# Kernel tuning notes

Measured on AMD Instinct MI355X. Metric: run time of the kernel, lower is better.

The kernel has to match this reference:

```python
import jax, jax.numpy as jnp
import numpy as np

N, E = 100000, 1600000
NF, HC, NC = 32, 64, 64


def setup_inputs() -> dict:
    key = jax.random.key(0)
    ks = jax.random.split(key, 12)
    s = 0.05
    return {
        "x": jax.random.normal(ks[0], (N, NF), dtype=jnp.float32),
        "edge_index": jax.random.randint(ks[1], (2, E), 0, N, dtype=jnp.int64),
        "eps1": jnp.float32(0.0),
        "eps2": jnp.float32(0.0),
        "W1a": jax.random.normal(ks[2], (NF, HC), dtype=jnp.float32) * s,
        "b1a": jnp.zeros((HC,), dtype=jnp.float32),
        "W1b": jax.random.normal(ks[3], (HC, HC), dtype=jnp.float32) * s,
        "b1b": jnp.zeros((HC,), dtype=jnp.float32),
        "W2a": jax.random.normal(ks[4], (HC, HC), dtype=jnp.float32) * s,
        "b2a": jnp.zeros((HC,), dtype=jnp.float32),
        "W2b": jax.random.normal(ks[5], (HC, NC), dtype=jnp.float32) * s,
        "b2b": jnp.zeros((NC,), dtype=jnp.float32),
    }


def _gin_conv(h, src, dst, eps, Wa, ba, Wb, bb, num_nodes):
    # sum-aggregate neighbor features: out[dst] += h[src]
    agg = jax.ops.segment_sum(h[src], dst, num_segments=num_nodes)
    z = (1.0 + eps) * h + agg
    # 2-layer MLP: Linear -> ReLU -> Linear
    z = jax.nn.relu(z @ Wa + ba)
    return z @ Wb + bb


def reference(x, edge_index, eps1, eps2, W1a, b1a, W1b, b1b, W2a, b2a, W2b, b2b):
    src, dst = edge_index[0], edge_index[1]
    n = x.shape[0]
    emb = _gin_conv(x, src, dst, eps1, W1a, b1a, W1b, b1b, n)  # [N, HC]
    h = jax.nn.relu(emb)  # dropout is identity in eval mode
    logits = _gin_conv(h, src, dst, eps2, W2a, b2a, W2b, b2b, n)  # [N, NC]
    return (logits, emb)
```

## Files before the change

### kernel.cpp

```cpp
#include <hip/hip_runtime.h>


#define NFEAT 32
#define HID   64
#define NCLS  64

#define BSH    6
#define BNODES 64
#define BCAP   2048
#define NBKT_LDS 2048

typedef unsigned int uint;
typedef unsigned short ushortT;
typedef __attribute__((ext_vector_type(8))) short bf16x8;
typedef __attribute__((ext_vector_type(4))) float f32x4;

__device__ __forceinline__ int clampi(int v, int hi){ v = v < 0 ? 0 : v; return v > hi ? hi : v; }

__device__ __forceinline__ ushortT f2b(float f){
  uint u = __float_as_uint(f);
  u = (u + 0x7FFFu + ((u >> 16) & 1u)) >> 16;
  return (ushortT)u;
}
__device__ __forceinline__ float b2f_lo(uint u){ return __uint_as_float(u << 16); }
__device__ __forceinline__ float b2f_hi(uint u){ return __uint_as_float(u & 0xFFFF0000u); }
__device__ __forceinline__ uint pack2(float lo, float hi){
  return (uint)f2b(lo) | ((uint)f2b(hi) << 16);
}


__global__ void k_prep(const float* __restrict__ x, ushortT* __restrict__ xb, int n4,
                       const float* __restrict__ W1a, const float* __restrict__ W1b,
                       const float* __restrict__ W2a, const float* __restrict__ W2b,
                       ushortT* __restrict__ T1a, ushortT* __restrict__ T1b,
                       ushortT* __restrict__ T2a, ushortT* __restrict__ T2b,
                       int* __restrict__ bktCnt, int nbkt){
  int t = blockIdx.x*256 + threadIdx.x;
  if (t < n4){
    float4 v = reinterpret_cast<const float4*>(x)[t];
    ushort4 o = { f2b(v.x), f2b(v.y), f2b(v.z), f2b(v.w) };
    reinterpret_cast<ushort4*>(xb)[t] = o;
  }
  if (t < nbkt) bktCnt[t] = 0;
  if (t < 14336){
    const float* W; ushortT* T; int K; int base;
    if      (t <  2048){ W=W1a; T=T1a; K=32; base=0;     }
    else if (t <  6144){ W=W1b; T=T1b; K=64; base=2048;  }
    else if (t < 10240){ W=W2a; T=T2a; K=64; base=6144;  }
    else               { W=W2b; T=T2b; K=64; base=10240; }
    int o = t - base;
    int k = o >> 6, c = o & 63;
    T[c*K + k] = f2b(W[o]);
  }
}


__global__ void k_bucket(const int* __restrict__ src, const int* __restrict__ dst,
                         int E, int N, int nbkt,
                         int* __restrict__ bktCnt, int* __restrict__ bktData){
  __shared__ int s_cnt[NBKT_LDS];
  __shared__ int s_base[NBKT_LDS];
  const int t = threadIdx.x;
  for (int j = t; j < nbkt; j += 256) s_cnt[j] = 0;
  __syncthreads();

  const int e0 = blockIdx.x * 4096;
  const int e1 = min(e0 + 4096, E);
  for (int e = e0 + t; e < e1; e += 256){
    int d = clampi(dst[e], N-1);
    atomicAdd(&s_cnt[d >> BSH], 1);
  }
  __syncthreads();
  for (int j = t; j < nbkt; j += 256){
    int c = s_cnt[j];
    s_base[j] = (c > 0) ? atomicAdd(&bktCnt[j], c) : 0;
    s_cnt[j] = 0;
  }
  __syncthreads();
  for (int e = e0 + t; e < e1; e += 256){
    int d = clampi(dst[e], N-1);
    int s = clampi(src[e], N-1);
    int b = d >> BSH;
    int p = s_base[b] + atomicAdd(&s_cnt[b], 1);
    if (p < BCAP)
      bktData[(size_t)b * BCAP + p] = ((d & (BNODES-1)) << 17) | s;
  }
}


template<int K, bool WRITE_HB>
__global__ __launch_bounds__(512)
void k_fused(const uint4* __restrict__ f4,
             const int* __restrict__ bktCnt, const int* __restrict__ bktData,
             const float* __restrict__ epsP,
             const ushortT* __restrict__ WaT,
             const float* __restrict__ ba,
             const ushortT* __restrict__ WbT,
             const float* __restrict__ bb,
             float* __restrict__ out,
             ushortT* __restrict__ hb, int N){
  constexpr int RS = K/8;
  constexpr int CH = RS/4;
  constexpr int U  = (CH == 1) ? 4 : 2;
  __shared__ int s_data[BCAP];
  __shared__ int s_eidx[BCAP];
  __shared__ int s_h[BNODES], s_cur[BNODES], s_row[BNODES+1];
  __shared__ __align__(16) ushortT zt[64*K];
  __shared__ __align__(16) ushortT ht[64*64];
  const int t = threadIdx.x;
  const int blk = blockIdx.x;
  const int row0 = blk * 64;

  const int cnt = min(bktCnt[blk], BCAP);
  const int* __restrict__ data = bktData + (size_t)blk * BCAP;
  if (t < BNODES) s_h[t] = 0;
  __syncthreads();
  for (int j = t; j < cnt; j += 512){
    int v = data[j];
    s_data[j] = v;
    atomicAdd(&s_h[v >> 17], 1);
  }
  __syncthreads();
  if (t < BNODES){
    int deg = s_h[t];
    int v = deg;
    #pragma unroll
    for (int off = 1; off < 64; off <<= 1){
      int u = __shfl_up(v, off);
      if (t >= off) v += u;
    }
    s_row[t+1] = v;
    if (t == 0) s_row[0] = 0;
    s_cur[t] = v - deg;
  }
  __syncthreads();
  for (int j = t; j < cnt; j += 512){
    int v = s_data[j];
    int p = atomicAdd(&s_cur[v >> 17], 1);
    s_eidx[p] = v & 0x1FFFF;
  }
  __syncthreads();

  {
    const int n = t >> 3;
    const int L = t & 7;
    const int q = L & 3;
    const int s = L >> 2;
    const int node = row0 + n;
    float acc[CH*8];
    #pragma unroll
    for (int j = 0; j < CH*8; ++j) acc[j] = 0.f;

    const int b = s_row[n];
    const int e = s_row[n+1];
    int i = b + s;
    for (; i + 2*(U-1) < e; i += 2*U){
      int src[U];
      #pragma unroll
      for (int u = 0; u < U; ++u) src[u] = s_eidx[i + 2*u];
      uint4 v[U][CH];
      #pragma unroll
      for (int u = 0; u < U; ++u)
        #pragma unroll
        for (int c = 0; c < CH; ++c)
          v[u][c] = f4[(size_t)src[u]*RS + q*CH + c];
      #pragma unroll
      for (int u = 0; u < U; ++u)
        #pragma unroll
        for (int c = 0; c < CH; ++c){
          acc[c*8+0] += b2f_lo(v[u][c].x); acc[c*8+1] += b2f_hi(v[u][c].x);
          acc[c*8+2] += b2f_lo(v[u][c].y); acc[c*8+3] += b2f_hi(v[u][c].y);
          acc[c*8+4] += b2f_lo(v[u][c].z); acc[c*8+5] += b2f_hi(v[u][c].z);
          acc[c*8+6] += b2f_lo(v[u][c].w); acc[c*8+7] += b2f_hi(v[u][c].w);
        }
    }
    for (; i < e; i += 2){
      int src0 = s_eidx[i];
      #pragma unroll
      for (int c = 0; c < CH; ++c){
        uint4 v = f4[(size_t)src0*RS + q*CH + c];
        acc[c*8+0] += b2f_lo(v.x); acc[c*8+1] += b2f_hi(v.x);
        acc[c*8+2] += b2f_lo(v.y); acc[c*8+3] += b2f_hi(v.y);
        acc[c*8+4] += b2f_lo(v.z); acc[c*8+5] += b2f_hi(v.z);
        acc[c*8+6] += b2f_lo(v.w); acc[c*8+7] += b2f_hi(v.w);
      }
    }
    if (s == 1 && node < N){
      const float se = 1.0f + epsP[0];
      #pragma unroll
      for (int c = 0; c < CH; ++c){
        uint4 v = f4[(size_t)node*RS + q*CH + c];
        acc[c*8+0] = fmaf(se, b2f_lo(v.x), acc[c*8+0]);
        acc[c*8+1] = fmaf(se, b2f_hi(v.x), acc[c*8+1]);
        acc[c*8+2] = fmaf(se, b2f_lo(v.y), acc[c*8+2]);
        acc[c*8+3] = fmaf(se, b2f_hi(v.y), acc[c*8+3]);
        acc[c*8+4] = fmaf(se, b2f_lo(v.z), acc[c*8+4]);
        acc[c*8+5] = fmaf(se, b2f_hi(v.z), acc[c*8+5]);
        acc[c*8+6] = fmaf(se, b2f_lo(v.w), acc[c*8+6]);
        acc[c*8+7] = fmaf(se, b2f_hi(v.w), acc[c*8+7]);
      }
    }
    #pragma unroll
    for (int j = 0; j < CH*8; ++j) acc[j] += __shfl_xor(acc[j], 4);
    if (s == 0){
      #pragma unroll
      for (int c = 0; c < CH; ++c){
        uint4 z;
        z.x = pack2(acc[c*8+0], acc[c*8+1]);
        z.y = pack2(acc[c*8+2], acc[c*8+3]);
        z.z = pack2(acc[c*8+4], acc[c*8+5]);
        z.w = pack2(acc[c*8+6], acc[c*8+7]);
        reinterpret_cast<uint4*>(zt)[n*RS + q*CH + c] = z;
      }
    }
  }
  __syncthreads();

  const int w  = t >> 6;
  const int l  = t & 63;
  const int lr = l & 15;
  const int lg = l >> 4;
  const int rf = w & 3;
  const int c0 = (w >> 2) * 2;
  f32x4 c1[2];
  #pragma unroll
  for (int cl = 0; cl < 2; ++cl){ float bv = ba[(c0+cl)*16 + lr]; c1[cl] = (f32x4){bv,bv,bv,bv}; }
  #pragma unroll
  for (int kf = 0; kf < K/32; ++kf){
    bf16x8 a = *reinterpret_cast<const bf16x8*>(&zt[(rf*16 + lr)*K + kf*32 + lg*8]);
    #pragma unroll
    for (int cl = 0; cl < 2; ++cl){
      bf16x8 bfr = *reinterpret_cast<const bf16x8*>(&WaT[((c0+cl)*16 + lr)*K + kf*32 + lg*8]);
      c1[cl] = __builtin_amdgcn_mfma_f32_16x16x32_bf16(a, bfr, c1[cl], 0, 0, 0);
    }
  }
  #pragma unroll
  for (int cl = 0; cl < 2; ++cl)
    #pragma unroll
    for (int r = 0; r < 4; ++r)
      ht[(rf*16 + lg*4 + r)*64 + (c0+cl)*16 + lr] = f2b(fmaxf(c1[cl][r], 0.f));
  __syncthreads();

  f32x4 c2[2];
  #pragma unroll
  for (int cl = 0; cl < 2; ++cl){ float bv = bb[(c0+cl)*16 + lr]; c2[cl] = (f32x4){bv,bv,bv,bv}; }
  #pragma unroll
  for (int kf = 0; kf < 2; ++kf){
    bf16x8 a = *reinterpret_cast<const bf16x8*>(&ht[(rf*16 + lr)*64 + kf*32 + lg*8]);
    #pragma unroll
    for (int cl = 0; cl < 2; ++cl){
      bf16x8 bfr = *reinterpret_cast<const bf16x8*>(&WbT[((c0+cl)*16 + lr)*64 + kf*32 + lg*8]);
      c2[cl] = __builtin_amdgcn_mfma_f32_16x16x32_bf16(a, bfr, c2[cl], 0, 0, 0);
    }
  }
  #pragma unroll
  for (int cl = 0; cl < 2; ++cl)
    #pragma unroll
    for (int r = 0; r < 4; ++r){
      int row = row0 + rf*16 + lg*4 + r;
      if (row < N){
        float v = c2[cl][r];
        out[(size_t)row*64 + (c0+cl)*16 + lr] = v;
        if (WRITE_HB) hb[(size_t)row*64 + (c0+cl)*16 + lr] = f2b(fmaxf(v, 0.f));
      }
    }
}


extern "C" void kernel_launch(void* const* d_in, const int* in_sizes, int n_in,
                              void* d_out, int out_size, void* d_ws, size_t ws_size,
                              hipStream_t stream) {
  const int N = in_sizes[0] / NFEAT;
  const int E = in_sizes[1] / 2;
  const int nbkt = (N + BNODES - 1) / BNODES;

  const float* x    = (const float*)d_in[0];
  const int*   ei   = (const int*)d_in[1];
  const int*   srcI = ei;
  const int*   dstI = ei + E;
  const float* eps1 = (const float*)d_in[2];
  const float* eps2 = (const float*)d_in[3];
  const float* W1a  = (const float*)d_in[4];
  const float* b1a  = (const float*)d_in[5];
  const float* W1b  = (const float*)d_in[6];
  const float* b1b  = (const float*)d_in[7];
  const float* W2a  = (const float*)d_in[8];
  const float* b2a  = (const float*)d_in[9];
  const float* W2b  = (const float*)d_in[10];
  const float* b2b  = (const float*)d_in[11];

  float* outLogits = (float*)d_out;
  float* outEmb    = outLogits + (size_t)N * HID;

  char* w = (char*)d_ws;
  size_t off = 0;
  auto alloc = [&](size_t bytes) -> void* {
    void* p = w + off;
    off = (off + bytes + 255) & ~(size_t)255;
    return p;
  };
  int*     bktCnt  = (int*)alloc((size_t)nbkt * sizeof(int));
  ushortT* T1a     = (ushortT*)alloc(64*32*sizeof(ushortT));
  ushortT* T1b     = (ushortT*)alloc(64*64*sizeof(ushortT));
  ushortT* T2a     = (ushortT*)alloc(64*64*sizeof(ushortT));
  ushortT* T2b     = (ushortT*)alloc(64*64*sizeof(ushortT));
  int*     bktData = (int*)alloc((size_t)nbkt * BCAP * sizeof(int));
  ushortT* xb      = (ushortT*)alloc((size_t)N * NFEAT * sizeof(ushortT));
  ushortT* hb      = (ushortT*)alloc((size_t)N * HID * sizeof(ushortT));

  const int n4 = N * NFEAT / 4;
  k_prep<<<(n4+255)/256, 256, 0, stream>>>(x, xb, n4, W1a, W1b, W2a, W2b,
                                           T1a, T1b, T2a, T2b, bktCnt, nbkt);

  k_bucket<<<(E+4095)/4096, 256, 0, stream>>>(srcI, dstI, E, N, nbkt, bktCnt, bktData);

  k_fused<NFEAT, true><<<nbkt, 512, 0, stream>>>((const uint4*)xb, bktCnt, bktData,
      eps1, T1a, b1a, T1b, b1b, outEmb, hb, N);

  k_fused<HID, false><<<nbkt, 512, 0, stream>>>((const uint4*)hb, bktCnt, bktData,
      eps2, T2a, b2a, T2b, b2b, outLogits, (ushortT*)nullptr, N);
}
```

Measured before the change: 119.5 us.

## Use coarse 512-node buckets with per-block octant filtering and padded LDS tiles

Buckets in k_bucket now cover 512 destination nodes, so there are far fewer of them (at most 256). Each fused block scans its whole bucket and keeps only the edges whose destination falls in its 64-node octant, using a wave ballot and a shared atomic to compact them. The aim is to cut global atomic contention and scattered writes during bucketing. The cost is that eight blocks each reread the same bucket window. LDS tiles for z and h also get padded row strides to reduce bank conflicts.

```diff
diff --git a/kernel.cpp b/kernel.cpp
--- a/kernel.cpp
+++ b/kernel.cpp
@@ -5,12 +5,14 @@
 #define HID   64
 #define NCLS  64
 
-#define BSH    6
-#define BNODES 64
-#define BCAP   2048
-#define NBKT_LDS 2048
+#define BSH   9
+#define BNODES 512
+#define NBKT_MAX 256
+#define BCAP  16384
+#define ECAP  2048
 
 typedef unsigned int uint;
+typedef unsigned long long ull;
 typedef unsigned short ushortT;
 typedef __attribute__((ext_vector_type(8))) short bf16x8;
 typedef __attribute__((ext_vector_type(4))) float f32x4;
@@ -58,8 +60,8 @@
 __global__ void k_bucket(const int* __restrict__ src, const int* __restrict__ dst,
                          int E, int N, int nbkt,
                          int* __restrict__ bktCnt, int* __restrict__ bktData){
-  __shared__ int s_cnt[NBKT_LDS];
-  __shared__ int s_base[NBKT_LDS];
+  __shared__ int s_cnt[NBKT_MAX];
+  __shared__ int s_base[NBKT_MAX];
   const int t = threadIdx.x;
   for (int j = t; j < nbkt; j += 256) s_cnt[j] = 0;
   __syncthreads();
@@ -102,26 +104,50 @@
   constexpr int RS = K/8;
   constexpr int CH = RS/4;
   constexpr int U  = (CH == 1) ? 4 : 2;
-  __shared__ int s_data[BCAP];
-  __shared__ int s_eidx[BCAP];
-  __shared__ int s_h[BNODES], s_cur[BNODES], s_row[BNODES+1];
-  __shared__ __align__(16) ushortT zt[64*K];
-  __shared__ __align__(16) ushortT ht[64*64];
+  constexpr int ZS = K + 8;
+  constexpr int HS = 72;
+  __shared__ int s_data[ECAP];
+  __shared__ int s_eidx[ECAP];
+  __shared__ int s_h[64], s_cur[64], s_row[65];
+  __shared__ int s_kept;
+  __shared__ __align__(16) ushortT zt[64*ZS];
+  __shared__ __align__(16) ushortT ht[64*HS];
   const int t = threadIdx.x;
-  const int blk = blockIdx.x;
-  const int row0 = blk * 64;
-
-  const int cnt = min(bktCnt[blk], BCAP);
-  const int* __restrict__ data = bktData + (size_t)blk * BCAP;
-  if (t < BNODES) s_h[t] = 0;
-  __syncthreads();
-  for (int j = t; j < cnt; j += 512){
-    int v = data[j];
-    s_data[j] = v;
-    atomicAdd(&s_h[v >> 17], 1);
-  }
-  __syncthreads();
-  if (t < BNODES){
+  const int bkt = blockIdx.x >> 3;
+  const int oct = blockIdx.x & 7;
+  const int row0 = blockIdx.x * 64;
+
+  const int cnt = min(bktCnt[bkt], BCAP);
+  const int* __restrict__ wnd = bktData + (size_t)bkt * BCAP;
+  if (t == 0) s_kept = 0;
+  if (t < 64) s_h[t] = 0;
+  __syncthreads();
+  {
+    const int lane = t & 63;
+    const int passes = (cnt + 511) >> 9;
+    for (int p = 0; p < passes; ++p){
+      int j = p*512 + t;
+      int v = (j < cnt) ? wnd[j] : 0;
+      bool m = (j < cnt) && (((v >> 23) & 7) == oct);
+      ull mask = __ballot(m);
+      int nkeep = __popcll(mask);
+      int pre   = __popcll(mask & ((lane ? (~0ull >> (64-lane)) : 0ull)));
+      int base0 = 0;
+      if (lane == 0 && nkeep) base0 = atomicAdd(&s_kept, nkeep);
+      base0 = __shfl(base0, 0);
+      if (m){
+        int p2 = base0 + pre;
+        if (p2 < ECAP){
+          s_data[p2] = v;
+          atomicAdd(&s_h[(v >> 17) & 63], 1);
+        }
+      }
+    }
+  }
+  __syncthreads();
+  const int kept = min(s_kept, ECAP);
+
+  if (t < 64){
     int deg = s_h[t];
     int v = deg;
     #pragma unroll
@@ -134,9 +160,9 @@
     s_cur[t] = v - deg;
   }
   __syncthreads();
-  for (int j = t; j < cnt; j += 512){
+  for (int j = t; j < kept; j += 512){
     int v = s_data[j];
-    int p = atomicAdd(&s_cur[v >> 17], 1);
+    int p = atomicAdd(&s_cur[(v >> 17) & 63], 1);
     s_eidx[p] = v & 0x1FFFF;
   }
   __syncthreads();
@@ -185,6 +211,7 @@
         acc[c*8+6] += b2f_lo(v.w); acc[c*8+7] += b2f_hi(v.w);
       }
     }
+
     if (s == 1 && node < N){
       const float se = 1.0f + epsP[0];
       #pragma unroll
@@ -210,7 +237,7 @@
         z.y = pack2(acc[c*8+2], acc[c*8+3]);
         z.z = pack2(acc[c*8+4], acc[c*8+5]);
         z.w = pack2(acc[c*8+6], acc[c*8+7]);
-        reinterpret_cast<uint4*>(zt)[n*RS + q*CH + c] = z;
+        *reinterpret_cast<uint4*>(&zt[n*ZS + (q*CH + c)*8]) = z;
       }
     }
   }
@@ -227,7 +254,7 @@
   for (int cl = 0; cl < 2; ++cl){ float bv = ba[(c0+cl)*16 + lr]; c1[cl] = (f32x4){bv,bv,bv,bv}; }
   #pragma unroll
   for (int kf = 0; kf < K/32; ++kf){
-    bf16x8 a = *reinterpret_cast<const bf16x8*>(&zt[(rf*16 + lr)*K + kf*32 + lg*8]);
+    bf16x8 a = *reinterpret_cast<const bf16x8*>(&zt[(rf*16 + lr)*ZS + kf*32 + lg*8]);
     #pragma unroll
     for (int cl = 0; cl < 2; ++cl){
       bf16x8 bfr = *reinterpret_cast<const bf16x8*>(&WaT[((c0+cl)*16 + lr)*K + kf*32 + lg*8]);
@@ -238,7 +265,7 @@
   for (int cl = 0; cl < 2; ++cl)
     #pragma unroll
     for (int r = 0; r < 4; ++r)
-      ht[(rf*16 + lg*4 + r)*64 + (c0+cl)*16 + lr] = f2b(fmaxf(c1[cl][r], 0.f));
+      ht[(rf*16 + lg*4 + r)*HS + (c0+cl)*16 + lr] = f2b(fmaxf(c1[cl][r], 0.f));
   __syncthreads();
 
   f32x4 c2[2];
@@ -246,7 +273,7 @@
   for (int cl = 0; cl < 2; ++cl){ float bv = bb[(c0+cl)*16 + lr]; c2[cl] = (f32x4){bv,bv,bv,bv}; }
   #pragma unroll
   for (int kf = 0; kf < 2; ++kf){
-    bf16x8 a = *reinterpret_cast<const bf16x8*>(&ht[(rf*16 + lr)*64 + kf*32 + lg*8]);
+    bf16x8 a = *reinterpret_cast<const bf16x8*>(&ht[(rf*16 + lr)*HS + kf*32 + lg*8]);
     #pragma unroll
     for (int cl = 0; cl < 2; ++cl){
       bf16x8 bfr = *reinterpret_cast<const bf16x8*>(&WbT[((c0+cl)*16 + lr)*64 + kf*32 + lg*8]);
@@ -299,12 +326,12 @@
     off = (off + bytes + 255) & ~(size_t)255;
     return p;
   };
-  int*     bktCnt  = (int*)alloc((size_t)nbkt * sizeof(int));
+  int*     bktCnt  = (int*)alloc((size_t)NBKT_MAX * sizeof(int));
   ushortT* T1a     = (ushortT*)alloc(64*32*sizeof(ushortT));
   ushortT* T1b     = (ushortT*)alloc(64*64*sizeof(ushortT));
   ushortT* T2a     = (ushortT*)alloc(64*64*sizeof(ushortT));
   ushortT* T2b     = (ushortT*)alloc(64*64*sizeof(ushortT));
-  int*     bktData = (int*)alloc((size_t)nbkt * BCAP * sizeof(int));
+  int*     bktData = (int*)alloc((size_t)NBKT_MAX * BCAP * sizeof(int));
   ushortT* xb      = (ushortT*)alloc((size_t)N * NFEAT * sizeof(ushortT));
   ushortT* hb      = (ushortT*)alloc((size_t)N * HID * sizeof(ushortT));
 
@@ -314,9 +341,10 @@
 
   k_bucket<<<(E+4095)/4096, 256, 0, stream>>>(srcI, dstI, E, N, nbkt, bktCnt, bktData);
 
-  k_fused<NFEAT, true><<<nbkt, 512, 0, stream>>>((const uint4*)xb, bktCnt, bktData,
+  const int nblk = nbkt * 8;
+  k_fused<NFEAT, true><<<nblk, 512, 0, stream>>>((const uint4*)xb, bktCnt, bktData,
       eps1, T1a, b1a, T1b, b1b, outEmb, hb, N);
 
-  k_fused<HID, false><<<nbkt, 512, 0, stream>>>((const uint4*)hb, bktCnt, bktData,
+  k_fused<HID, false><<<nblk, 512, 0, stream>>>((const uint4*)hb, bktCnt, bktData,
       eps2, T2a, b2a, T2b, b2b, outLogits, (ushortT*)nullptr, N);
 }
```

After: 137.9 us. +15.4%, slower.
